# Kernel optimization log

Measured on AMD Instinct MI355X. Metric: run time of the kernel, lower is better.

The kernel has to match this reference:

```python
import jax, jax.numpy as jnp
import numpy as np

DIM = 64
N_GRAPHS = 300
N_NODES = 12000
N_EDGES = 40000


def setup_inputs() -> dict:
    key = jax.random.key(0)
    ks = jax.random.split(key, 16)
    N, E, F_IN, D = N_NODES, N_EDGES, 14, DIM

    def w(k, shape, fan_in):
        return jax.random.normal(k, shape, dtype=jnp.float32) / np.float32(np.sqrt(fan_in))

    return {
        "x": jax.random.normal(ks[0], (N, F_IN), dtype=jnp.float32),
        "edge_index": jax.random.randint(ks[1], (2, E), 0, N),
        "edge_attr": jax.random.uniform(ks[2], (E, 4), dtype=jnp.float32),
        "batch": jnp.sort(jax.random.randint(ks[3], (N,), 0, N_GRAPHS)),
        # lin0
        "lin0_w": w(ks[4], (D, F_IN), F_IN), "lin0_b": jnp.zeros((D,), jnp.float32),
        # edge MLP: Linear(4,128) -> ReLU -> Linear(128, D*D)
        "nn1_w": w(ks[5], (128, 4), 4), "nn1_b": jnp.zeros((128,), jnp.float32),
        "nn2_w": w(ks[6], (D * D, 128), 128), "nn2_b": jnp.zeros((D * D,), jnp.float32),
        # NNConv root weight + bias
        "root_w": w(ks[7], (D, D), D), "conv_b": jnp.zeros((D,), jnp.float32),
        # GRU(D, D), gate order r,z,n
        "gru_w_ih": w(ks[8], (3 * D, D), D), "gru_w_hh": w(ks[9], (3 * D, D), D),
        "gru_b_ih": jnp.zeros((3 * D,), jnp.float32), "gru_b_hh": jnp.zeros((3 * D,), jnp.float32),
        # Set2Set LSTM(2D -> D), gate order i,f,g,o
        "lstm_w_ih": w(ks[10], (4 * D, 2 * D), 2 * D), "lstm_w_hh": w(ks[11], (4 * D, D), D),
        "lstm_b_ih": jnp.zeros((4 * D,), jnp.float32), "lstm_b_hh": jnp.zeros((4 * D,), jnp.float32),
        # readout
        "lin1_w": w(ks[12], (D, 2 * D), 2 * D), "lin1_b": jnp.zeros((D,), jnp.float32),
        "lin2_w": w(ks[13], (1, D), D), "lin2_b": jnp.zeros((1,), jnp.float32),
    }


def _mpnn_forward(x, edge_index, edge_attr, batch,
                  lin0_w, lin0_b, nn1_w, nn1_b, nn2_w, nn2_b, root_w, conv_b,
                  gru_w_ih, gru_w_hh, gru_b_ih, gru_b_hh,
                  lstm_w_ih, lstm_w_hh, lstm_b_ih, lstm_b_hh,
                  lin1_w, lin1_b, lin2_w, lin2_b):
    N, D, B = x.shape[0], DIM, N_GRAPHS
    src, dst = edge_index[0], edge_index[1]

    out = jax.nn.relu(x @ lin0_w.T + lin0_b)          # [N, D]
    h = out

    # per-edge weight matrices from edge MLP: [E, D, D]
    W_e = (jax.nn.relu(edge_attr @ nn1_w.T + nn1_b) @ nn2_w.T + nn2_b).reshape(-1, D, D)
    deg = jnp.maximum(
        jax.ops.segment_sum(jnp.ones(src.shape, x.dtype), dst, num_segments=N), 1.0)

    for _ in range(3):
        # NNConv: gather -> per-edge bmm -> scatter-mean, plus root term and bias
        msg = jnp.einsum('ei,eio->eo', out[src], W_e)                 # [E, D]
        agg = jax.ops.segment_sum(msg, dst, num_segments=N) / deg[:, None]
        m = jax.nn.relu(out @ root_w + agg + conv_b)
        # GRU cell (torch gate order r, z, n)
        gx = m @ gru_w_ih.T + gru_b_ih
        gh = h @ gru_w_hh.T + gru_b_hh
        r = jax.nn.sigmoid(gx[:, :D] + gh[:, :D])
        z = jax.nn.sigmoid(gx[:, D:2 * D] + gh[:, D:2 * D])
        n = jnp.tanh(gx[:, 2 * D:] + r * gh[:, 2 * D:])
        h = (1.0 - z) * n + z * h
        out = h

    per_atom_out = out

    # Set2Set pooling, 3 processing steps
    q_star = jnp.zeros((B, 2 * D), x.dtype)
    hs = jnp.zeros((B, D), x.dtype)
    cs = jnp.zeros((B, D), x.dtype)
    for _ in range(3):
        gates = q_star @ lstm_w_ih.T + lstm_b_ih + hs @ lstm_w_hh.T + lstm_b_hh
        i_g = jax.nn.sigmoid(gates[:, 0 * D:1 * D])
        f_g = jax.nn.sigmoid(gates[:, 1 * D:2 * D])
        g_g = jnp.tanh(gates[:, 2 * D:3 * D])
        o_g = jax.nn.sigmoid(gates[:, 3 * D:4 * D])
        cs = f_g * cs + i_g * g_g
        hs = o_g * jnp.tanh(cs)
        q = hs                                                         # [B, D]
        e = jnp.sum(out * q[batch], axis=-1)                           # [N]
        e_max = jax.ops.segment_max(e, batch, num_segments=B)
        a = jnp.exp(e - e_max[batch])
        a = a / jax.ops.segment_sum(a, batch, num_segments=B)[batch]   # scatter-softmax
        r_read = jax.ops.segment_sum(a[:, None] * out, batch, num_segments=B)
        q_star = jnp.concatenate([q, r_read], axis=-1)                 # [B, 2D]

    y = jax.nn.relu(q_star @ lin1_w.T + lin1_b)
    y = (y @ lin2_w.T + lin2_b).reshape(-1)                            # [B]
    return (y, per_atom_out)


def reference(x, edge_index, edge_attr, batch,
              lin0_w, lin0_b, nn1_w, nn1_b, nn2_w, nn2_b, root_w, conv_b,
              gru_w_ih, gru_w_hh, gru_b_ih, gru_b_hh,
              lstm_w_ih, lstm_w_hh, lstm_b_ih, lstm_b_hh,
              lin1_w, lin1_b, lin2_w, lin2_b):
    return _mpnn_forward(x, edge_index, edge_attr, batch,
                         lin0_w, lin0_b, nn1_w, nn1_b, nn2_w, nn2_b, root_w, conv_b,
                         gru_w_ih, gru_w_hh, gru_b_ih, gru_b_hh,
                         lstm_w_ih, lstm_w_hh, lstm_b_ih, lstm_b_hh,
                         lin1_w, lin1_b, lin2_w, lin2_b)
```

## Files before the change

kernel.cpp:

```cpp
#include <hip/hip_runtime.h>
#include <math.h>

#define NBG 300
#define KP 8256

typedef __attribute__((ext_vector_type(8))) short short8_t;
typedef __attribute__((ext_vector_type(4))) float f32x4_t;

#define MFMA16(a,b,c) __builtin_amdgcn_mfma_f32_16x16x32_bf16(a,b,c,0,0,0)

__device__ __forceinline__ float sigmoidf_(float x){ return 1.0f/(1.0f+expf(-x)); }
__device__ __forceinline__ float bf2f(short s){
  union{unsigned u; float f;} v; v.u = ((unsigned)(unsigned short)s) << 16; return v.f;
}
__device__ __forceinline__ short f2bf(float f){
  union{float f; unsigned u;} v; v.f = f;
  unsigned r = (v.u + 0x7fffu + ((v.u >> 16) & 1u)) >> 16;
  return (short)r;
}
__device__ __forceinline__ unsigned cvt_pk_bf16(float lo, float hi){
  unsigned r;
  asm volatile("v_cvt_pk_bf16_f32 %0, %1, %2" : "=v"(r) : "v"(lo), "v"(hi));
  return r;
}
union FragA { short8_t v; unsigned u[4]; };

__global__ void lin0_kernel(const float* __restrict__ x, const float* __restrict__ w,
                            const float* __restrict__ b, float* __restrict__ out,
                            short* __restrict__ out_bf, int N){
  int n = blockIdx.x; int d = threadIdx.x;
  __shared__ float xs[16];
  if (d < 14) xs[d] = x[n*14 + d];
  __syncthreads();
  float acc = b[d];
  #pragma unroll
  for (int k = 0; k < 14; ++k) acc = fmaf(xs[k], w[d*14 + k], acc);
  float v = fmaxf(acc, 0.0f);
  out[n*64 + d] = v;
  out_bf[n*64 + d] = f2bf(v);
}

__global__ void ehid_kernel(const float* __restrict__ ea, const float* __restrict__ w,
                            const float* __restrict__ b, short* __restrict__ hid_bf, int E){
  int e = blockIdx.x; int t = threadIdx.x;
  __shared__ float as[4];
  if (t < 4) as[t] = ea[e*4 + t];
  __syncthreads();
  float acc = b[t];
  #pragma unroll
  for (int k = 0; k < 4; ++k) acc = fmaf(as[k], w[t*4 + k], acc);
  hid_bf[(size_t)e*128 + t] = f2bf(fmaxf(acc, 0.0f));
}

__global__ void count_kernel(const int* __restrict__ idx, int* __restrict__ counts, int len){
  int e = blockIdx.x*blockDim.x + threadIdx.x;
  if (e < len) atomicAdd(&counts[idx[e]], 1);
}

__global__ __launch_bounds__(1024) void scan_kernel(const int* __restrict__ counts,
    int* __restrict__ starts, int* __restrict__ cursor, int N){
  __shared__ int part[1024];
  int t = threadIdx.x;
  int per = (N + 1023) >> 10;
  int base = t * per;
  int s = 0;
  for (int j = 0; j < per; ++j){ int idx = base + j; if (idx < N) s += counts[idx]; }
  part[t] = s;
  __syncthreads();
  for (int off = 1; off < 1024; off <<= 1){
    int v = (t >= off) ? part[t - off] : 0;
    __syncthreads();
    part[t] += v;
    __syncthreads();
  }
  int run = (t == 0) ? 0 : part[t-1];
  for (int j = 0; j < per; ++j){
    int idx = base + j;
    if (idx < N){ starts[idx] = run; cursor[idx] = run; run += counts[idx]; }
  }
}

__global__ void scatter_kernel(const int* __restrict__ dst, int* __restrict__ cursor,
                               int* __restrict__ sorted_eid, int E){
  int e = blockIdx.x*blockDim.x + threadIdx.x;
  if (e < E){ int p = atomicAdd(&cursor[dst[e]], 1); sorted_eid[p] = e; }
}

__global__ void w2t_build(const float* __restrict__ w2, const float* __restrict__ b2,
                          short* __restrict__ W2t){
  int o = blockIdx.x;
  for (int k = threadIdx.x; k < KP; k += blockDim.x){
    float val;
    if (k < 8192){ int i = k >> 7, h = k & 127; val = w2[(size_t)(i*64 + o)*128 + h]; }
    else val = b2[(k - 8192)*64 + o];
    W2t[(size_t)o*KP + k] = f2bf(val);
  }
}

__global__ __launch_bounds__(256) void msg_gemm2(
    const short* __restrict__ out_bf, const short* __restrict__ hid_bf,
    const short* __restrict__ W2t, const int* __restrict__ sorted,
    const int* __restrict__ src, const int* __restrict__ dstv,
    float* __restrict__ agg, int E)
{
  __shared__ float sS[64][72];
  __shared__ __align__(16) unsigned char bufB[2][4096];
  __shared__ int eid_s[64];
  __shared__ int dst_s[64];

  const int tid = threadIdx.x;
  const int blk = blockIdx.x;
  const int split = blockIdx.y;

  if (tid < 64){
    int p = blk*64 + tid;
    int e = (p < E) ? sorted[p] : -1;
    eid_s[tid] = e;
    dst_s[tid] = (e >= 0) ? dstv[e] : -1;
  }
  __syncthreads();

  {
    int er = tid >> 2, kq = tid & 3;
    int e = eid_s[er];
    if (e >= 0){
      const short* sp = out_bf + (size_t)src[e]*64 + kq*16;
      short8_t v0 = *(const short8_t*)(sp);
      short8_t v1 = *(const short8_t*)(sp + 8);
      #pragma unroll
      for (int j = 0; j < 8; ++j){
        sS[er][kq*16 + j]     = bf2f(v0[j]);
        sS[er][kq*16 + 8 + j] = bf2f(v1[j]);
      }
    } else {
      #pragma unroll
      for (int j = 0; j < 16; ++j) sS[er][kq*16 + j] = 0.f;
    }
  }

  const int lane = tid & 63, wid = tid >> 6;
  const int r = lane & 15, q4 = lane >> 4;
  const int mh = wid * 16;
  const int eloc = mh + r;

  float hq0[8], hq1[8], hq2[8], hq3[8];
  {
    int e = eid_s[eloc];
    if (e >= 0){
      const short* hp = hid_bf + (size_t)e*128 + q4*8;
      short8_t v0 = *(const short8_t*)(hp);
      short8_t v1 = *(const short8_t*)(hp + 32);
      short8_t v2 = *(const short8_t*)(hp + 64);
      short8_t v3 = *(const short8_t*)(hp + 96);
      #pragma unroll
      for (int j = 0; j < 8; ++j){
        hq0[j] = bf2f(v0[j]); hq1[j] = bf2f(v1[j]);
        hq2[j] = bf2f(v2[j]); hq3[j] = bf2f(v3[j]);
      }
    } else {
      #pragma unroll
      for (int j = 0; j < 8; ++j){ hq0[j]=0.f; hq1[j]=0.f; hq2[j]=0.f; hq3[j]=0.f; }
    }
  }

  const int o_st = tid >> 2, kq_st = tid & 3;
  const int swz_st = kq_st ^ (o_st & 3);
  const uint4* w2p = (const uint4*)(W2t + (size_t)o_st*KP);
  const unsigned stoff = (unsigned)(o_st*64 + swz_st*16);

  int boff0, boff1, boff2, boff3;
  {
    int o0 = r, o1 = 16 + r, o2 = 32 + r, o3 = 48 + r;
    boff0 = o0*64 + ((q4 ^ (o0 & 3))*16);
    boff1 = o1*64 + ((q4 ^ (o1 & 3))*16);
    boff2 = o2*64 + ((q4 ^ (o2 & 3))*16);
    boff3 = o3*64 + ((q4 ^ (o3 & 3))*16);
  }

  const int cstart = split * 128;
  const int cend   = split ? 258 : 128;
  int c = cstart;
  uint4 gvA = w2p[(size_t)c*4 + kq_st];
  uint4 gvB = w2p[(size_t)(c+1)*4 + kq_st];

  f32x4_t z4 = {0.f,0.f,0.f,0.f};
  f32x4_t acc0 = z4, acc1 = z4, acc2 = z4, acc3 = z4;
  int ph = 0;
  const int ibase = split * 32;

  __syncthreads();

#define MSG_CHUNK(HQ)                                                   \
  {                                                                     \
    *(uint4*)(bufB[ph] + stoff) = gvA;                                  \
    gvA = gvB;                                                          \
    __syncthreads();                                                    \
    {int nc2 = (c + 2 < cend) ? (c + 2) : (cend - 1);                   \
     gvB = w2p[(size_t)nc2*4 + kq_st];}                                 \
    short8_t b0 = *(const short8_t*)(bufB[ph] + boff0);                 \
    short8_t b1 = *(const short8_t*)(bufB[ph] + boff1);                 \
    short8_t b2 = *(const short8_t*)(bufB[ph] + boff2);                 \
    short8_t b3 = *(const short8_t*)(bufB[ph] + boff3);                 \
    FragA fa;                                                           \
    fa.u[0] = cvt_pk_bf16(sv*HQ[0], sv*HQ[1]);                         \
    fa.u[1] = cvt_pk_bf16(sv*HQ[2], sv*HQ[3]);                         \
    fa.u[2] = cvt_pk_bf16(sv*HQ[4], sv*HQ[5]);                         \
    fa.u[3] = cvt_pk_bf16(sv*HQ[6], sv*HQ[7]);                         \
    acc0 = MFMA16(fa.v, b0, acc0);                                      \
    acc1 = MFMA16(fa.v, b1, acc1);                                      \
    acc2 = MFMA16(fa.v, b2, acc2);                                      \
    acc3 = MFMA16(fa.v, b3, acc3);                                      \
    ph ^= 1; ++c;                                                       \
  }

  #pragma unroll 1
  for (int q = 0; q < 32; ++q){
    float sv = sS[eloc][ibase + q];
    MSG_CHUNK(hq0)
    MSG_CHUNK(hq1)
    MSG_CHUNK(hq2)
    MSG_CHUNK(hq3)
  }

  if (split){
    #pragma unroll 1
    for (int bc = 0; bc < 2; ++bc){
      *(uint4*)(bufB[ph] + stoff) = gvA;
      gvA = gvB;
      __syncthreads();
      {int nc2 = (c + 2 < cend) ? (c + 2) : (cend - 1);
       gvB = w2p[(size_t)nc2*4 + kq_st];}
      short8_t b0 = *(const short8_t*)(bufB[ph] + boff0);
      short8_t b1 = *(const short8_t*)(bufB[ph] + boff1);
      short8_t b2 = *(const short8_t*)(bufB[ph] + boff2);
      short8_t b3 = *(const short8_t*)(bufB[ph] + boff3);
      const float* sp = &sS[eloc][(c - 256)*32 + q4*8];
      float4 s0 = *(const float4*)(sp);
      float4 s1 = *(const float4*)(sp + 4);
      FragA fa;
      fa.u[0] = cvt_pk_bf16(s0.x, s0.y);
      fa.u[1] = cvt_pk_bf16(s0.z, s0.w);
      fa.u[2] = cvt_pk_bf16(s1.x, s1.y);
      fa.u[3] = cvt_pk_bf16(s1.z, s1.w);
      acc0 = MFMA16(fa.v, b0, acc0);
      acc1 = MFMA16(fa.v, b1, acc1);
      acc2 = MFMA16(fa.v, b2, acc2);
      acc3 = MFMA16(fa.v, b3, acc3);
      ph ^= 1; ++c;
    }
  }

  {
    int ebase = mh + q4*4;
    float c0 = 0.f, c1 = 0.f, c2 = 0.f, c3 = 0.f;
    #pragma unroll
    for (int reg = 0; reg < 4; ++reg){
      c0 += acc0[reg]; c1 += acc1[reg]; c2 += acc2[reg]; c3 += acc3[reg];
      int d = dst_s[ebase + reg];
      int dn = (reg < 3) ? dst_s[ebase + reg + 1] : -2;
      if (d != dn){
        if (d >= 0){
          float* ap = agg + (size_t)d*64;
          atomicAdd(ap + r,      c0);
          atomicAdd(ap + 16 + r, c1);
          atomicAdd(ap + 32 + r, c2);
          atomicAdd(ap + 48 + r, c3);
        }
        c0 = c1 = c2 = c3 = 0.f;
      }
    }
  }
}

__global__ __launch_bounds__(256) void node_mfma(
    const short* __restrict__ out_bf, const float* __restrict__ agg,
    const int* __restrict__ counts,
    const float* __restrict__ root_w, const float* __restrict__ conv_b,
    const float* __restrict__ gwih, const float* __restrict__ gwhh,
    const float* __restrict__ gbih, const float* __restrict__ gbhh,
    float* __restrict__ out, short* __restrict__ out_bf_w,
    float* __restrict__ out_dup, int N)
{
  __shared__ short XH[64*128];
  __shared__ short rootT[64*64];
  __shared__ short Wih_s[192*64];
  __shared__ short Whh_s[192*64];
  __shared__ float rdeg_s[64];
  __shared__ float cb_s[64];

  int tid = threadIdx.x;
  int blk = blockIdx.x;
  int nbase = blk*64;

  {
    int n = tid >> 2, cq = tid & 3;
    int ng = nbase + n;
    short8_t v0 = {0,0,0,0,0,0,0,0}, v1 = v0;
    if (ng < N){
      const short* p = out_bf + (size_t)ng*64;
      v0 = *(const short8_t*)(p + cq*16);
      v1 = *(const short8_t*)(p + cq*16 + 8);
    }
    int c0 = 8 + cq*2;
    *(short8_t*)(XH + n*128 + ((c0     ^ (n & 7))*8)) = v0;
    *(short8_t*)(XH + n*128 + (((c0+1) ^ (n & 7))*8)) = v1;
  }
  {
    int i = tid >> 2, dq = tid & 3;
    #pragma unroll
    for (int j = 0; j < 16; ++j){
      int d = dq*16 + j;
      short v = f2bf(root_w[i*64 + d]);
      rootT[d*64 + (((i >> 3) ^ (d & 7))*8) + (i & 7)] = v;
    }
  }
  if (tid < 192){
    int g = tid;
    short pk[8];
    #pragma unroll
    for (int c = 0; c < 8; ++c){
      #pragma unroll
      for (int j = 0; j < 8; ++j) pk[j] = f2bf(gwih[g*64 + c*8 + j]);
      *(short8_t*)(Wih_s + g*64 + ((c ^ (g & 7))*8)) = *(short8_t*)&pk[0];
    }
    #pragma unroll
    for (int c = 0; c < 8; ++c){
      #pragma unroll
      for (int j = 0; j < 8; ++j) pk[j] = f2bf(gwhh[g*64 + c*8 + j]);
      *(short8_t*)(Whh_s + g*64 + ((c ^ (g & 7))*8)) = *(short8_t*)&pk[0];
    }
  }
  if (tid < 64){
    int ng = nbase + tid;
    int c = (ng < N) ? counts[ng] : 1;
    rdeg_s[tid] = 1.0f / fmaxf((float)c, 1.0f);
    cb_s[tid] = conv_b[tid];
  }
  __syncthreads();

  int lane = tid & 63, wid = tid >> 6;
  int r = lane & 15, q4 = lane >> 4;

  {
    int mh = (wid >> 1)*32, nh = (wid & 1)*32;
    f32x4_t z4 = {0.f,0.f,0.f,0.f};
    f32x4_t c00 = z4, c01 = z4, c10 = z4, c11 = z4;
    #pragma unroll
    for (int ks = 0; ks < 2; ++ks){
      int ck = 8 + ks*4 + q4;
      int swA = (ck ^ (r & 7))*8;
      int swB = ((ks*4 + q4) ^ (r & 7))*8;
      short8_t a0 = *(const short8_t*)(XH + (mh + r)*128 + swA);
      short8_t a1 = *(const short8_t*)(XH + (mh + 16 + r)*128 + swA);
      short8_t b0 = *(const short8_t*)(rootT + (nh + r)*64 + swB);
      short8_t b1 = *(const short8_t*)(rootT + (nh + 16 + r)*64 + swB);
      c00 = MFMA16(a0, b0, c00);
      c01 = MFMA16(a0, b1, c01);
      c10 = MFMA16(a1, b0, c10);
      c11 = MFMA16(a1, b1, c11);
    }
    #pragma unroll
    for (int mm = 0; mm < 2; ++mm){
      #pragma unroll
      for (int nn = 0; nn < 2; ++nn){
        f32x4_t cc = mm == 0 ? (nn == 0 ? c00 : c01) : (nn == 0 ? c10 : c11);
        int d = nh + nn*16 + r;
        #pragma unroll
        for (int reg = 0; reg < 4; ++reg){
          int n = mh + mm*16 + q4*4 + reg;
          int ng = nbase + n;
          float av = (ng < N) ? agg[(size_t)ng*64 + d] : 0.0f;
          float v = cc[reg] + av * rdeg_s[n] + cb_s[d];
          v = fmaxf(v, 0.0f);
          XH[n*128 + (((d >> 3) ^ (n & 7))*8) + (d & 7)] = f2bf(v);
        }
      }
    }
  }
  __syncthreads();

  f32x4_t ax[4][3], ah[4][3];
  {
    f32x4_t z4 = {0.f,0.f,0.f,0.f};
    #pragma unroll
    for (int mt = 0; mt < 4; ++mt)
      #pragma unroll
      for (int gt = 0; gt < 3; ++gt){ ax[mt][gt] = z4; ah[mt][gt] = z4; }
  }
  #pragma unroll
  for (int ks = 0; ks < 2; ++ks){
    int ckM = ks*4 + q4;
    int ckH = 8 + ks*4 + q4;
    int swM = (ckM ^ (r & 7))*8;
    int swH = (ckH ^ (r & 7))*8;
    int swB = ((ks*4 + q4) ^ (r & 7))*8;
    short8_t bx[3], bh[3];
    #pragma unroll
    for (int gt = 0; gt < 3; ++gt){
      int g = gt*64 + wid*16 + r;
      bx[gt] = *(const short8_t*)(Wih_s + g*64 + swB);
      bh[gt] = *(const short8_t*)(Whh_s + g*64 + swB);
    }
    #pragma unroll
    for (int mt = 0; mt < 4; ++mt){
      short8_t aM = *(const short8_t*)(XH + (mt*16 + r)*128 + swM);
      short8_t aH = *(const short8_t*)(XH + (mt*16 + r)*128 + swH);
      #pragma unroll
      for (int gt = 0; gt < 3; ++gt){
        ax[mt][gt] = MFMA16(aM, bx[gt], ax[mt][gt]);
        ah[mt][gt] = MFMA16(aH, bh[gt], ah[mt][gt]);
      }
    }
  }

  {
    int d = wid*16 + r;
    float bir = gbih[d],      bhr = gbhh[d];
    float biz = gbih[64 + d], bhz = gbhh[64 + d];
    float bin_ = gbih[128 + d], bhn = gbhh[128 + d];
    #pragma unroll
    for (int mt = 0; mt < 4; ++mt){
      #pragma unroll
      for (int reg = 0; reg < 4; ++reg){
        int n = mt*16 + q4*4 + reg;
        int ng = nbase + n;
        if (ng < N){
          float gxr = ax[mt][0][reg], gxz = ax[mt][1][reg], gxn = ax[mt][2][reg];
          float ghr = ah[mt][0][reg], ghz = ah[mt][1][reg], ghn = ah[mt][2][reg];
          float rr = sigmoidf_(gxr + ghr + bir + bhr);
          float zz = sigmoidf_(gxz + ghz + biz + bhz);
          float nn = tanhf(gxn + bin_ + rr*(ghn + bhn));
          float h = out[(size_t)ng*64 + d];
          float v = (1.0f - zz)*nn + zz*h;
          out[(size_t)ng*64 + d] = v;
          out_bf_w[(size_t)ng*64 + d] = f2bf(v);
          if (out_dup) out_dup[(size_t)ng*64 + d] = v;
        }
      }
    }
  }
}

__global__ __launch_bounds__(256) void set2set_kernel(
    const float* __restrict__ out, const int* __restrict__ bstarts,
    const int* __restrict__ bcounts,
    const float* __restrict__ lwih, const float* __restrict__ lwhh,
    const float* __restrict__ lbih, const float* __restrict__ lbhh,
    const float* __restrict__ l1w, const float* __restrict__ l1b,
    const float* __restrict__ l2w, const float* __restrict__ l2b,
    float* __restrict__ y)
{
  int b = blockIdx.x, t = threadIdx.x;
  int lane = t & 63, wid = t >> 6;
  __shared__ float qs[128];
  __shared__ float hsl[64], hs_s[64], cs_s[64];
  __shared__ float ev[512];
  __shared__ float red[256];
  __shared__ float rpart[4][64];
  __shared__ float scal[2];

  int s0 = bstarts[b], cnt = bcounts[b];
  if (cnt > 512) cnt = 512;
  if (t < 64){ hs_s[t] = 0.f; cs_s[t] = 0.f; }
  if (t < 128) qs[t] = 0.f;
  __syncthreads();

  for (int step = 0; step < 3; ++step){
    if (t < 64) hsl[t] = hs_s[t];
    __syncthreads();
    {
      float a0 = lbih[t] + lbhh[t], a1 = 0.f, a2 = 0.f, a3 = 0.f;
      const float* wi = lwih + t*128;
      #pragma unroll
      for (int kq = 0; kq < 32; ++kq){
        float4 w4 = *(const float4*)(wi + kq*4);
        a0 = fmaf(qs[kq*4+0], w4.x, a0);
        a1 = fmaf(qs[kq*4+1], w4.y, a1);
        a2 = fmaf(qs[kq*4+2], w4.z, a2);
        a3 = fmaf(qs[kq*4+3], w4.w, a3);
      }
      const float* wh = lwhh + t*64;
      #pragma unroll
      for (int kq = 0; kq < 16; ++kq){
        float4 w4 = *(const float4*)(wh + kq*4);
        a0 = fmaf(hsl[kq*4+0], w4.x, a0);
        a1 = fmaf(hsl[kq*4+1], w4.y, a1);
        a2 = fmaf(hsl[kq*4+2], w4.z, a2);
        a3 = fmaf(hsl[kq*4+3], w4.w, a3);
      }
      red[t] = (a0 + a1) + (a2 + a3);
    }
    __syncthreads();
    if (t < 64){
      float ig = sigmoidf_(red[t]);
      float fg = sigmoidf_(red[64 + t]);
      float gg = tanhf(red[128 + t]);
      float og = sigmoidf_(red[192 + t]);
      float c = fg*cs_s[t] + ig*gg;
      cs_s[t] = c;
      hs_s[t] = og*tanhf(c);
    }
    __syncthreads();

    float lmax = -1e30f;
    for (int idx = t; idx < cnt; idx += 256){
      const float* row = out + (size_t)(s0 + idx)*64;
      float a0 = 0.f, a1 = 0.f, a2 = 0.f, a3 = 0.f;
      #pragma unroll
      for (int kq = 0; kq < 16; ++kq){
        float4 v = *(const float4*)(row + kq*4);
        a0 = fmaf(v.x, hs_s[kq*4+0], a0);
        a1 = fmaf(v.y, hs_s[kq*4+1], a1);
        a2 = fmaf(v.z, hs_s[kq*4+2], a2);
        a3 = fmaf(v.w, hs_s[kq*4+3], a3);
      }
      float acc = (a0 + a1) + (a2 + a3);
      ev[idx] = acc;
      lmax = fmaxf(lmax, acc);
    }
    red[t] = lmax;
    __syncthreads();
    #pragma unroll
    for (int off = 128; off > 0; off >>= 1){
      if (t < off) red[t] = fmaxf(red[t], red[t + off]);
      __syncthreads();
    }
    if (t == 0) scal[0] = red[0];
    __syncthreads();
    float m = scal[0];

    float ls = 0.f;
    for (int idx = t; idx < cnt; idx += 256){
      float a = expf(ev[idx] - m);
      ev[idx] = a;
      ls += a;
    }
    red[t] = ls;
    __syncthreads();
    #pragma unroll
    for (int off = 128; off > 0; off >>= 1){
      if (t < off) red[t] += red[t + off];
      __syncthreads();
    }
    if (t == 0) scal[1] = red[0];
    __syncthreads();
    float lst = scal[1];

    float part = 0.f;
    for (int idx = wid; idx < cnt; idx += 4)
      part = fmaf(ev[idx], out[(size_t)(s0 + idx)*64 + lane], part);
    rpart[wid][lane] = part;
    __syncthreads();
    if (t < 64){
      float r = (rpart[0][t] + rpart[1][t]) + (rpart[2][t] + rpart[3][t]);
      r = (cnt > 0) ? r / lst : 0.f;
      qs[t] = hs_s[t];
      qs[64 + t] = r;
    }
    __syncthreads();
  }

  if (t < 64){
    float a0 = l1b[t], a1 = 0.f, a2 = 0.f, a3 = 0.f;
    const float* w1 = l1w + t*128;
    #pragma unroll
    for (int kq = 0; kq < 32; ++kq){
      float4 w4 = *(const float4*)(w1 + kq*4);
      a0 = fmaf(qs[kq*4+0], w4.x, a0);
      a1 = fmaf(qs[kq*4+1], w4.y, a1);
      a2 = fmaf(qs[kq*4+2], w4.z, a2);
      a3 = fmaf(qs[kq*4+3], w4.w, a3);
    }
    float acc = (a0 + a1) + (a2 + a3);
    float v = fmaxf(acc, 0.0f) * l2w[t];
    #pragma unroll
    for (int off = 32; off > 0; off >>= 1) v += __shfl_xor(v, off, 64);
    if (t == 0) y[b] = v + l2b[0];
  }
}

extern "C" void kernel_launch(void* const* d_in, const int* in_sizes, int n_in,
                              void* d_out, int out_size, void* d_ws, size_t ws_size,
                              hipStream_t stream){
  const float* x      = (const float*)d_in[0];
  const int*   ei     = (const int*)  d_in[1];
  const float* ea     = (const float*)d_in[2];
  const int*   batch  = (const int*)  d_in[3];
  const float* lin0_w = (const float*)d_in[4];
  const float* lin0_b = (const float*)d_in[5];
  const float* nn1_w  = (const float*)d_in[6];
  const float* nn1_b  = (const float*)d_in[7];
  const float* nn2_w  = (const float*)d_in[8];
  const float* nn2_b  = (const float*)d_in[9];
  const float* root_w = (const float*)d_in[10];
  const float* conv_b = (const float*)d_in[11];
  const float* gwih   = (const float*)d_in[12];
  const float* gwhh   = (const float*)d_in[13];
  const float* gbih   = (const float*)d_in[14];
  const float* gbhh   = (const float*)d_in[15];
  const float* lwih   = (const float*)d_in[16];
  const float* lwhh   = (const float*)d_in[17];
  const float* lbih   = (const float*)d_in[18];
  const float* lbhh   = (const float*)d_in[19];
  const float* l1w    = (const float*)d_in[20];
  const float* l1b    = (const float*)d_in[21];
  const float* l2w    = (const float*)d_in[22];
  const float* l2b    = (const float*)d_in[23];

  const int N = in_sizes[0] / 14;
  const int E = in_sizes[1] / 2;
  const int B = NBG;
  const int* src  = ei;
  const int* dstv = ei + E;

  char* wsp = (char*)d_ws; size_t off = 0;
  auto alloc = [&](size_t bytes)->char* {
    char* p = wsp + off; off += (bytes + 255) & ~((size_t)255); return p;
  };
  float* out     = (float*)alloc((size_t)N*64*4);
  short* out_bf  = (short*)alloc((size_t)N*64*2);
  float* agg     = (float*)alloc((size_t)N*64*4);
  int*   counts  = (int*)  alloc((size_t)N*4);
  int*   starts  = (int*)  alloc((size_t)N*4);
  int*   cursor  = (int*)  alloc((size_t)N*4);
  int*   sorted  = (int*)  alloc((size_t)E*4);
  int*   bcounts = (int*)  alloc((size_t)B*4);
  int*   bstarts = (int*)  alloc((size_t)B*4);
  int*   bcursor = (int*)  alloc((size_t)B*4);
  short* hid_bf  = (short*)alloc((size_t)E*128*2);
  short* W2t     = (short*)alloc((size_t)64*KP*2);

  lin0_kernel<<<N, 64, 0, stream>>>(x, lin0_w, lin0_b, out, out_bf, N);
  ehid_kernel<<<E, 128, 0, stream>>>(ea, nn1_w, nn1_b, hid_bf, E);

  hipMemsetAsync(counts, 0, (size_t)N*4, stream);
  count_kernel<<<(E + 255)/256, 256, 0, stream>>>(dstv, counts, E);
  scan_kernel<<<1, 1024, 0, stream>>>(counts, starts, cursor, N);
  scatter_kernel<<<(E + 255)/256, 256, 0, stream>>>(dstv, cursor, sorted, E);

  hipMemsetAsync(bcounts, 0, (size_t)B*4, stream);
  count_kernel<<<(N + 255)/256, 256, 0, stream>>>(batch, bcounts, N);
  scan_kernel<<<1, 1024, 0, stream>>>(bcounts, bstarts, bcursor, B);

  w2t_build<<<64, 256, 0, stream>>>(nn2_w, nn2_b, W2t);

  int mblocks = (E + 63)/64;
  int nblocks = (N + 63)/64;
  dim3 mg(mblocks, 2);
  for (int it = 0; it < 3; ++it){
    hipMemsetAsync(agg, 0, (size_t)N*64*4, stream);
    msg_gemm2<<<mg, 256, 0, stream>>>(out_bf, hid_bf, W2t, sorted, src, dstv, agg, E);
    node_mfma<<<nblocks, 256, 0, stream>>>(out_bf, agg, counts, root_w, conv_b,
                                           gwih, gwhh, gbih, gbhh, out, out_bf,
                                           (it == 2) ? ((float*)d_out + 300) : nullptr, N);
  }

  set2set_kernel<<<B, 256, 0, stream>>>(out, bstarts, bcounts, lwih, lwhh, lbih, lbhh,
                                        l1w, l1b, l2w, l2b, (float*)d_out);
}
```

Baseline: 386.1 us.

## Double edge tile per block and stream W2 via direct global-to-LDS loads

The message GEMM now processes 128 edges per block (two 16-row MFMA tiles per wave), so each W2 chunk loaded into LDS is reused across twice as many edges. W2 chunks are fetched with global_load_lds into a 4-deep ring buffer using explicit waitcnt plus barrier instead of register staging, and the source features and hidden activations stay in bf16, unpacked on the fly. This halves W2 traffic per edge and shortens the load pipeline, at the cost of more accumulator registers, fewer blocks, and delicate hand-written synchronisation.

```diff
diff --git a/kernel.cpp b/kernel.cpp
--- a/kernel.cpp
+++ b/kernel.cpp
@@ -24,6 +24,18 @@
   return r;
 }
 union FragA { short8_t v; unsigned u[4]; };
+
+__device__ __forceinline__ short8_t frag_from(float sv, short8_t h){
+  union { short8_t v; unsigned u[4]; } hh; hh.v = h;
+  FragA fa;
+  #pragma unroll
+  for (int k2 = 0; k2 < 4; ++k2){
+    float lo = __uint_as_float(hh.u[k2] << 16);
+    float hi = __uint_as_float(hh.u[k2] & 0xffff0000u);
+    fa.u[k2] = cvt_pk_bf16(sv*lo, sv*hi);
+  }
+  return fa.v;
+}
 
 __global__ void lin0_kernel(const float* __restrict__ x, const float* __restrict__ w,
                             const float* __restrict__ b, float* __restrict__ out,
@@ -97,165 +109,167 @@
   }
 }
 
-__global__ __launch_bounds__(256) void msg_gemm2(
+__global__ __launch_bounds__(256) void msg_gemm3(
     const short* __restrict__ out_bf, const short* __restrict__ hid_bf,
     const short* __restrict__ W2t, const int* __restrict__ sorted,
     const int* __restrict__ src, const int* __restrict__ dstv,
     float* __restrict__ agg, int E)
 {
-  __shared__ float sS[64][72];
-  __shared__ __align__(16) unsigned char bufB[2][4096];
-  __shared__ int eid_s[64];
-  __shared__ int dst_s[64];
+  __shared__ short sSb[128*80];
+  __shared__ __align__(16) char bufB[4][4096];
+  __shared__ int eid_s[128];
+  __shared__ int dst_s[128];
 
   const int tid = threadIdx.x;
   const int blk = blockIdx.x;
   const int split = blockIdx.y;
 
-  if (tid < 64){
-    int p = blk*64 + tid;
+  if (tid < 128){
+    int p = blk*128 + tid;
     int e = (p < E) ? sorted[p] : -1;
     eid_s[tid] = e;
     dst_s[tid] = (e >= 0) ? dstv[e] : -1;
   }
   __syncthreads();
 
-  {
-    int er = tid >> 2, kq = tid & 3;
-    int e = eid_s[er];
-    if (e >= 0){
-      const short* sp = out_bf + (size_t)src[e]*64 + kq*16;
-      short8_t v0 = *(const short8_t*)(sp);
-      short8_t v1 = *(const short8_t*)(sp + 8);
-      #pragma unroll
-      for (int j = 0; j < 8; ++j){
-        sS[er][kq*16 + j]     = bf2f(v0[j]);
-        sS[er][kq*16 + 8 + j] = bf2f(v1[j]);
-      }
-    } else {
-      #pragma unroll
-      for (int j = 0; j < 16; ++j) sS[er][kq*16 + j] = 0.f;
-    }
-  }
-
   const int lane = tid & 63, wid = tid >> 6;
   const int r = lane & 15, q4 = lane >> 4;
-  const int mh = wid * 16;
-  const int eloc = mh + r;
-
-  float hq0[8], hq1[8], hq2[8], hq3[8];
-  {
-    int e = eid_s[eloc];
+  const int eloc0 = wid*32 + r;
+  const int eloc1 = eloc0 + 16;
+
+  short8_t z8 = {0,0,0,0,0,0,0,0};
+
+  {
+    int row = tid >> 1, half = tid & 1;
+    int e = eid_s[row];
+    short* dp = sSb + row*80 + half*32;
     if (e >= 0){
-      const short* hp = hid_bf + (size_t)e*128 + q4*8;
-      short8_t v0 = *(const short8_t*)(hp);
-      short8_t v1 = *(const short8_t*)(hp + 32);
-      short8_t v2 = *(const short8_t*)(hp + 64);
-      short8_t v3 = *(const short8_t*)(hp + 96);
-      #pragma unroll
-      for (int j = 0; j < 8; ++j){
-        hq0[j] = bf2f(v0[j]); hq1[j] = bf2f(v1[j]);
-        hq2[j] = bf2f(v2[j]); hq3[j] = bf2f(v3[j]);
-      }
+      const short* sp = out_bf + (size_t)src[e]*64 + half*32;
+      *(short8_t*)(dp)      = *(const short8_t*)(sp);
+      *(short8_t*)(dp + 8)  = *(const short8_t*)(sp + 8);
+      *(short8_t*)(dp + 16) = *(const short8_t*)(sp + 16);
+      *(short8_t*)(dp + 24) = *(const short8_t*)(sp + 24);
     } else {
-      #pragma unroll
-      for (int j = 0; j < 8; ++j){ hq0[j]=0.f; hq1[j]=0.f; hq2[j]=0.f; hq3[j]=0.f; }
-    }
-  }
-
-  const int o_st = tid >> 2, kq_st = tid & 3;
-  const int swz_st = kq_st ^ (o_st & 3);
-  const uint4* w2p = (const uint4*)(W2t + (size_t)o_st*KP);
-  const unsigned stoff = (unsigned)(o_st*64 + swz_st*16);
+      *(short8_t*)(dp) = z8; *(short8_t*)(dp + 8) = z8;
+      *(short8_t*)(dp + 16) = z8; *(short8_t*)(dp + 24) = z8;
+    }
+  }
+
+  short8_t hq0_0=z8, hq0_1=z8, hq0_2=z8, hq0_3=z8;
+  short8_t hq1_0=z8, hq1_1=z8, hq1_2=z8, hq1_3=z8;
+  {
+    int e0 = eid_s[eloc0], e1 = eid_s[eloc1];
+    if (e0 >= 0){
+      const short* hp = hid_bf + (size_t)e0*128 + q4*8;
+      hq0_0 = *(const short8_t*)(hp);      hq0_1 = *(const short8_t*)(hp + 32);
+      hq0_2 = *(const short8_t*)(hp + 64); hq0_3 = *(const short8_t*)(hp + 96);
+    }
+    if (e1 >= 0){
+      const short* hp = hid_bf + (size_t)e1*128 + q4*8;
+      hq1_0 = *(const short8_t*)(hp);      hq1_1 = *(const short8_t*)(hp + 32);
+      hq1_2 = *(const short8_t*)(hp + 64); hq1_3 = *(const short8_t*)(hp + 96);
+    }
+  }
+
+  const int gl_o  = tid >> 2;
+  const int gl_kq = (tid & 3) ^ ((tid >> 3) & 3);
+  const char* w2b = (const char*)W2t;
+  const size_t gbase = (size_t)gl_o*(KP*2) + (size_t)gl_kq*16;
 
   int boff0, boff1, boff2, boff3;
   {
     int o0 = r, o1 = 16 + r, o2 = 32 + r, o3 = 48 + r;
-    boff0 = o0*64 + ((q4 ^ (o0 & 3))*16);
-    boff1 = o1*64 + ((q4 ^ (o1 & 3))*16);
-    boff2 = o2*64 + ((q4 ^ (o2 & 3))*16);
-    boff3 = o3*64 + ((q4 ^ (o3 & 3))*16);
-  }
-
+    boff0 = (o0*4 + (q4 ^ ((o0 >> 1) & 3))) * 16;
+    boff1 = (o1*4 + (q4 ^ ((o1 >> 1) & 3))) * 16;
+    boff2 = (o2*4 + (q4 ^ ((o2 >> 1) & 3))) * 16;
+    boff3 = (o3*4 + (q4 ^ ((o3 >> 1) & 3))) * 16;
+  }
+
+  const int nc     = split ? 130 : 128;
   const int cstart = split * 128;
-  const int cend   = split ? 258 : 128;
-  int c = cstart;
-  uint4 gvA = w2p[(size_t)c*4 + kq_st];
-  uint4 gvB = w2p[(size_t)(c+1)*4 + kq_st];
-
-  f32x4_t z4 = {0.f,0.f,0.f,0.f};
-  f32x4_t acc0 = z4, acc1 = z4, acc2 = z4, acc3 = z4;
-  int ph = 0;
-  const int ibase = split * 32;
-
-  __syncthreads();
-
-#define MSG_CHUNK(HQ)                                                   \
-  {                                                                     \
-    *(uint4*)(bufB[ph] + stoff) = gvA;                                  \
-    gvA = gvB;                                                          \
-    __syncthreads();                                                    \
-    {int nc2 = (c + 2 < cend) ? (c + 2) : (cend - 1);                   \
-     gvB = w2p[(size_t)nc2*4 + kq_st];}                                 \
-    short8_t b0 = *(const short8_t*)(bufB[ph] + boff0);                 \
-    short8_t b1 = *(const short8_t*)(bufB[ph] + boff1);                 \
-    short8_t b2 = *(const short8_t*)(bufB[ph] + boff2);                 \
-    short8_t b3 = *(const short8_t*)(bufB[ph] + boff3);                 \
-    FragA fa;                                                           \
-    fa.u[0] = cvt_pk_bf16(sv*HQ[0], sv*HQ[1]);                         \
-    fa.u[1] = cvt_pk_bf16(sv*HQ[2], sv*HQ[3]);                         \
-    fa.u[2] = cvt_pk_bf16(sv*HQ[4], sv*HQ[5]);                         \
-    fa.u[3] = cvt_pk_bf16(sv*HQ[6], sv*HQ[7]);                         \
-    acc0 = MFMA16(fa.v, b0, acc0);                                      \
-    acc1 = MFMA16(fa.v, b1, acc1);                                      \
-    acc2 = MFMA16(fa.v, b2, acc2);                                      \
-    acc3 = MFMA16(fa.v, b3, acc3);                                      \
-    ph ^= 1; ++c;                                                       \
+  const int clast  = cstart + nc - 1;
+
+#define GLOAD(c_, bi_)                                                          \
+  __builtin_amdgcn_global_load_lds(                                             \
+      (const __attribute__((address_space(1))) unsigned*)(w2b + gbase + (size_t)(c_)*64), \
+      (__attribute__((address_space(3))) unsigned*)(&bufB[bi_][wid*1024]), 16, 0, 0)
+
+  GLOAD(cstart + 0, (cstart + 0) & 3);
+  GLOAD(cstart + 1, (cstart + 1) & 3);
+  GLOAD(cstart + 2, (cstart + 2) & 3);
+  __syncthreads();
+
+  f32x4_t zz = {0.f,0.f,0.f,0.f};
+  f32x4_t acc00 = zz, acc01 = zz, acc02 = zz, acc03 = zz;
+  f32x4_t acc10 = zz, acc11 = zz, acc12 = zz, acc13 = zz;
+
+#define CHUNK(QI, Q, HQ0, HQ1)                                                  \
+  {                                                                             \
+    int c = cstart + (QI)*4 + (Q);                                              \
+    asm volatile("s_waitcnt vmcnt(2) lgkmcnt(0)" ::: "memory");                 \
+    __builtin_amdgcn_s_barrier();                                               \
+    const char* bp = bufB[c & 3];                                               \
+    short8_t b0 = *(const short8_t*)(bp + boff0);                               \
+    short8_t b1 = *(const short8_t*)(bp + boff1);                               \
+    short8_t b2 = *(const short8_t*)(bp + boff2);                               \
+    short8_t b3 = *(const short8_t*)(bp + boff3);                               \
+    { int cn = c + 3; if (cn > clast) cn = clast; GLOAD(cn, (c + 3) & 3); }     \
+    short8_t f0 = frag_from(sv0, HQ0);                                          \
+    short8_t f1 = frag_from(sv1, HQ1);                                          \
+    acc00 = MFMA16(f0, b0, acc00);                                              \
+    acc01 = MFMA16(f0, b1, acc01);                                              \
+    acc02 = MFMA16(f0, b2, acc02);                                              \
+    acc03 = MFMA16(f0, b3, acc03);                                              \
+    acc10 = MFMA16(f1, b0, acc10);                                              \
+    acc11 = MFMA16(f1, b1, acc11);                                              \
+    acc12 = MFMA16(f1, b2, acc12);                                              \
+    acc13 = MFMA16(f1, b3, acc13);                                              \
   }
 
   #pragma unroll 1
-  for (int q = 0; q < 32; ++q){
-    float sv = sS[eloc][ibase + q];
-    MSG_CHUNK(hq0)
-    MSG_CHUNK(hq1)
-    MSG_CHUNK(hq2)
-    MSG_CHUNK(hq3)
+  for (int qi = 0; qi < 32; ++qi){
+    int qg = (split << 5) + qi;
+    float sv0 = bf2f(sSb[eloc0*80 + qg]);
+    float sv1 = bf2f(sSb[eloc1*80 + qg]);
+    CHUNK(qi, 0, hq0_0, hq1_0)
+    CHUNK(qi, 1, hq0_1, hq1_1)
+    CHUNK(qi, 2, hq0_2, hq1_2)
+    CHUNK(qi, 3, hq0_3, hq1_3)
   }
 
   if (split){
-    #pragma unroll 1
-    for (int bc = 0; bc < 2; ++bc){
-      *(uint4*)(bufB[ph] + stoff) = gvA;
-      gvA = gvB;
-      __syncthreads();
-      {int nc2 = (c + 2 < cend) ? (c + 2) : (cend - 1);
-       gvB = w2p[(size_t)nc2*4 + kq_st];}
-      short8_t b0 = *(const short8_t*)(bufB[ph] + boff0);
-      short8_t b1 = *(const short8_t*)(bufB[ph] + boff1);
-      short8_t b2 = *(const short8_t*)(bufB[ph] + boff2);
-      short8_t b3 = *(const short8_t*)(bufB[ph] + boff3);
-      const float* sp = &sS[eloc][(c - 256)*32 + q4*8];
-      float4 s0 = *(const float4*)(sp);
-      float4 s1 = *(const float4*)(sp + 4);
-      FragA fa;
-      fa.u[0] = cvt_pk_bf16(s0.x, s0.y);
-      fa.u[1] = cvt_pk_bf16(s0.z, s0.w);
-      fa.u[2] = cvt_pk_bf16(s1.x, s1.y);
-      fa.u[3] = cvt_pk_bf16(s1.z, s1.w);
-      acc0 = MFMA16(fa.v, b0, acc0);
-      acc1 = MFMA16(fa.v, b1, acc1);
-      acc2 = MFMA16(fa.v, b2, acc2);
-      acc3 = MFMA16(fa.v, b3, acc3);
-      ph ^= 1; ++c;
-    }
-  }
-
-  {
-    int ebase = mh + q4*4;
+    #pragma unroll
+    for (int tc = 0; tc < 2; ++tc){
+      int c = 256 + tc;
+      asm volatile("s_waitcnt vmcnt(2) lgkmcnt(0)" ::: "memory");
+      __builtin_amdgcn_s_barrier();
+      const char* bp = bufB[c & 3];
+      short8_t b0 = *(const short8_t*)(bp + boff0);
+      short8_t b1 = *(const short8_t*)(bp + boff1);
+      short8_t b2 = *(const short8_t*)(bp + boff2);
+      short8_t b3 = *(const short8_t*)(bp + boff3);
+      GLOAD(clast, (c + 3) & 3);
+      short8_t f0 = *(const short8_t*)(sSb + eloc0*80 + tc*32 + q4*8);
+      short8_t f1 = *(const short8_t*)(sSb + eloc1*80 + tc*32 + q4*8);
+      acc00 = MFMA16(f0, b0, acc00);
+      acc01 = MFMA16(f0, b1, acc01);
+      acc02 = MFMA16(f0, b2, acc02);
+      acc03 = MFMA16(f0, b3, acc03);
+      acc10 = MFMA16(f1, b0, acc10);
+      acc11 = MFMA16(f1, b1, acc11);
+      acc12 = MFMA16(f1, b2, acc12);
+      acc13 = MFMA16(f1, b3, acc13);
+    }
+  }
+
+  asm volatile("s_waitcnt vmcnt(0)" ::: "memory");
+
+  {
+    int ebase = wid*32 + q4*4;
     float c0 = 0.f, c1 = 0.f, c2 = 0.f, c3 = 0.f;
     #pragma unroll
     for (int reg = 0; reg < 4; ++reg){
-      c0 += acc0[reg]; c1 += acc1[reg]; c2 += acc2[reg]; c3 += acc3[reg];
+      c0 += acc00[reg]; c1 += acc01[reg]; c2 += acc02[reg]; c3 += acc03[reg];
       int d = dst_s[ebase + reg];
       int dn = (reg < 3) ? dst_s[ebase + reg + 1] : -2;
       if (d != dn){
@@ -270,6 +284,28 @@
       }
     }
   }
+  {
+    int ebase = wid*32 + 16 + q4*4;
+    float c0 = 0.f, c1 = 0.f, c2 = 0.f, c3 = 0.f;
+    #pragma unroll
+    for (int reg = 0; reg < 4; ++reg){
+      c0 += acc10[reg]; c1 += acc11[reg]; c2 += acc12[reg]; c3 += acc13[reg];
+      int d = dst_s[ebase + reg];
+      int dn = (reg < 3) ? dst_s[ebase + reg + 1] : -2;
+      if (d != dn){
+        if (d >= 0){
+          float* ap = agg + (size_t)d*64;
+          atomicAdd(ap + r,      c0);
+          atomicAdd(ap + 16 + r, c1);
+          atomicAdd(ap + 32 + r, c2);
+          atomicAdd(ap + 48 + r, c3);
+        }
+        c0 = c1 = c2 = c3 = 0.f;
+      }
+    }
+  }
+#undef CHUNK
+#undef GLOAD
 }
 
 __global__ __launch_bounds__(256) void node_mfma(
@@ -644,12 +680,12 @@
 
   w2t_build<<<64, 256, 0, stream>>>(nn2_w, nn2_b, W2t);
 
-  int mblocks = (E + 63)/64;
+  int mblocks = (E + 127)/128;
   int nblocks = (N + 63)/64;
   dim3 mg(mblocks, 2);
   for (int it = 0; it < 3; ++it){
     hipMemsetAsync(agg, 0, (size_t)N*64*4, stream);
-    msg_gemm2<<<mg, 256, 0, stream>>>(out_bf, hid_bf, W2t, sorted, src, dstv, agg, E);
+    msg_gemm3<<<mg, 256, 0, stream>>>(out_bf, hid_bf, W2t, sorted, src, dstv, agg, E);
     node_mfma<<<nblocks, 256, 0, stream>>>(out_bf, agg, counts, root_w, conv_b,
                                            gwih, gwhh, gbih, gbhh, out, out_bf,
                                            (it == 2) ? ((float*)d_out + 300) : nullptr, N);
```

New measurement: 388.6 us. About the same (+0.6%).
